# Kernel optimization log

Measured on AMD Instinct MI355X. Metric: run time of the kernel, lower is better.

Reference implementation:

```python
import jax, jax.numpy as jnp
import numpy as np

B, N, K, H = 4, 2048, 30, 128
NODE_IN, EDGE_IN, FF = 21, 16, 4 * H


def _normalize(t, axis=-1):
    d = t / jnp.linalg.norm(t, axis=axis, keepdims=True)
    return jnp.where(jnp.isnan(d), 0.0, d)


def gather_nodes(nodes, idx):
    # nodes: [B,N,C], idx: [B,N,K] -> [B,N,K,C]
    b, n, k = idx.shape
    flat = idx.reshape(b, n * k)
    out = jnp.take_along_axis(nodes, flat[:, :, None], axis=1)
    return out.reshape(b, n, k, nodes.shape[-1])


def cal_dihedral(Xf, eps=1e-7):
    dX = Xf[:, 1:, :] - Xf[:, :-1, :]
    U = _normalize(dX)
    u0, u1, u2 = U[:, :-2], U[:, 1:-1], U[:, 2:]
    n0 = _normalize(jnp.cross(u0, u1))
    n1 = _normalize(jnp.cross(u1, u2))
    cosD = jnp.clip((n0 * n1).sum(-1), -1 + eps, 1 - eps)
    v = _normalize(jnp.cross(n0, n1))
    return jnp.sign((-v * u1).sum(-1)) * jnp.arccos(cosD)


def dihedrals(X, eps=1e-7):
    b, n = X.shape[0], X.shape[1]
    Xf = X[:, :, :3, :].reshape(b, 3 * n, 3)
    D = cal_dihedral(Xf)
    D = jnp.pad(D, ((0, 0), (1, 2))).reshape(b, n, 3)
    dihed = jnp.concatenate([jnp.cos(D), jnp.sin(D)], -1)
    dX = Xf[:, 1:] - Xf[:, :-1]
    U = _normalize(dX)
    cosA = jnp.clip((U[:, :-2] * U[:, 1:-1]).sum(-1), -1 + eps, 1 - eps)
    A = jnp.pad(jnp.arccos(cosA), ((0, 0), (1, 2))).reshape(b, n, 3)
    ang = jnp.concatenate([jnp.cos(A), jnp.sin(A)], -1)
    return jnp.concatenate([dihed, ang], -1)  # [B,N,12]


def quaternions(R):
    diag = jnp.diagonal(R, axis1=-2, axis2=-1)
    Rxx, Ryy, Rzz = diag[..., 0], diag[..., 1], diag[..., 2]
    mags = 0.5 * jnp.sqrt(jnp.abs(1 + jnp.stack([Rxx - Ryy - Rzz, -Rxx + Ryy - Rzz, -Rxx - Ryy + Rzz], -1)))
    signs = jnp.sign(jnp.stack([R[..., 2, 1] - R[..., 1, 2], R[..., 0, 2] - R[..., 2, 0], R[..., 1, 0] - R[..., 0, 1]], -1))
    xyz = signs * mags
    w = jnp.sqrt(jax.nn.relu(1 + diag.sum(-1, keepdims=True))) / 2.0
    return _normalize(jnp.concatenate([xyz, w], -1))


def orientations(X, E_idx):
    V = X  # [B,N,4,3]
    b, n = X.shape[0], X.shape[1]
    k = E_idx.shape[2]
    Xf = X[:, :, :3, :].reshape(b, 3 * n, 3)
    dX = Xf[:, 1:] - Xf[:, :-1]
    U = _normalize(dX)
    u0, u1 = U[:, :-2], U[:, 1:-1]
    n0 = _normalize(jnp.cross(u0, u1))[:, ::3]
    b1 = _normalize(u0 - u1)[:, ::3]
    Xa = Xf[:, ::3]  # [B,N,3]
    Q = jnp.stack([b1, n0, jnp.cross(b1, n0)], 2)  # [B,N-1,3,3]
    Q = Q.reshape(b, Q.shape[1], 9)
    Q = jnp.pad(Q, ((0, 0), (0, 1), (0, 0)))  # [B,N,9]
    Qn = gather_nodes(Q, E_idx).reshape(b, n, k, 3, 3)
    Xn = gather_nodes(V[:, :, 1, :], E_idx)
    Nn = gather_nodes(V[:, :, 0, :], E_idx)
    Cn = gather_nodes(V[:, :, 2, :], E_idx)
    On = gather_nodes(V[:, :, 3, :], E_idx)
    Q3 = Q.reshape(b, n, 3, 3)
    dXn = jnp.stack([Xn, Nn, Cn, On], 3) - Xa[:, :, None, None, :]  # [B,N,K,4,3]
    dU = jnp.einsum('bnij,bnkaj->bnkai', Q3, dXn)
    E_direct = _normalize(dU).reshape(b, n, k, 12)
    R = jnp.einsum('bnji,bnkjl->bnkil', Q3, Qn)  # Q^T @ Q_neighbors
    q = quaternions(R)  # [B,N,K,4]
    dX_inner = V[:, :, jnp.array([0, 2, 3]), :] - Xa[:, :, None, :]
    dU_inner = _normalize(jnp.einsum('bnij,bnaj->bnai', Q3, dX_inner))
    V_direct = dU_inner.reshape(b, n, 9)
    return V_direct, E_direct, q


def layernorm(x, g, bta, eps=1e-5):
    m = x.mean(-1, keepdims=True)
    v = ((x - m) ** 2).mean(-1, keepdims=True)
    return (x - m) / jnp.sqrt(v + eps) * g + bta


def gelu(x):
    return jax.nn.gelu(x, approximate=False)


def forward(X, E_idx, Wv_w, Wv_b, We_w, We_b, W1_w, W1_b, W2_w, W2_b, W3_w, W3_b,
            Wi_w, Wi_b, Wo_w, Wo_b, ln1_g, ln1_b, ln2_g, ln2_b):
    k = E_idx.shape[2]
    Dfeat = dihedrals(X)                     # [B,N,12]
    Vd, Ed, q = orientations(X, E_idx)       # [B,N,9],[B,N,K,12],[B,N,K,4]
    hV = jnp.concatenate([Dfeat, Vd], -1) @ Wv_w + Wv_b     # [B,N,H]
    hE = jnp.concatenate([Ed, q], -1) @ We_w + We_b         # [B,N,K,H]
    hV_nbr = gather_nodes(hV, E_idx)                        # [B,N,K,H]
    hV_exp = jnp.broadcast_to(hV[:, :, None, :], hV_nbr.shape)
    hEV = jnp.concatenate([hV_exp, hE, hV_nbr], -1)         # [B,N,K,3H]
    msg = gelu(hEV @ W1_w + W1_b)
    msg = gelu(msg @ W2_w + W2_b)
    msg = msg @ W3_w + W3_b
    dh = msg.sum(-2) / k
    hV = layernorm(hV + dh, ln1_g, ln1_b)
    ff = gelu(hV @ Wi_w + Wi_b) @ Wo_w + Wo_b
    hV = layernorm(hV + ff, ln2_g, ln2_b)
    return hV


def _lin(key, fan_in, fan_out):
    s = 1.0 / np.sqrt(fan_in)
    kw, kb = jax.random.split(key)
    return (jax.random.uniform(kw, (fan_in, fan_out), minval=-s, maxval=s),
            jax.random.uniform(kb, (fan_out,), minval=-s, maxval=s))


def setup_inputs() -> dict:
    key = jax.random.key(0)
    ks = jax.random.split(key, 10)
    X = jax.random.normal(ks[0], (B, N, 4, 3), dtype=jnp.float32) * 3.0
    E_idx = jax.random.randint(ks[1], (B, N, K), 0, N)
    Wv_w, Wv_b = _lin(ks[2], NODE_IN, H)
    We_w, We_b = _lin(ks[3], EDGE_IN, H)
    W1_w, W1_b = _lin(ks[4], 3 * H, H)
    W2_w, W2_b = _lin(ks[5], H, H)
    W3_w, W3_b = _lin(ks[6], H, H)
    Wi_w, Wi_b = _lin(ks[7], H, FF)
    Wo_w, Wo_b = _lin(ks[8], FF, H)
    return {
        'X': X, 'E_idx': E_idx,
        'Wv_w': Wv_w, 'Wv_b': Wv_b, 'We_w': We_w, 'We_b': We_b,
        'W1_w': W1_w, 'W1_b': W1_b, 'W2_w': W2_w, 'W2_b': W2_b,
        'W3_w': W3_w, 'W3_b': W3_b, 'Wi_w': Wi_w, 'Wi_b': Wi_b,
        'Wo_w': Wo_w, 'Wo_b': Wo_b,
        'ln1_g': jnp.ones((H,), jnp.float32), 'ln1_b': jnp.zeros((H,), jnp.float32),
        'ln2_g': jnp.ones((H,), jnp.float32), 'ln2_b': jnp.zeros((H,), jnp.float32),
    }


def reference(X, E_idx, Wv_w, Wv_b, We_w, We_b, W1_w, W1_b, W2_w, W2_b, W3_w, W3_b,
              Wi_w, Wi_b, Wo_w, Wo_b, ln1_g, ln1_b, ln2_g, ln2_b):
    return forward(X, E_idx, Wv_w, Wv_b, We_w, We_b, W1_w, W1_b, W2_w, W2_b,
                   W3_w, W3_b, Wi_w, Wi_b, Wo_w, Wo_b, ln1_g, ln1_b, ln2_g, ln2_b)
```

## Files before the change

### kernel.cpp

```cpp
#include <hip/hip_runtime.h>
#include <math.h>

#define BB 4
#define NN 2048
#define KNB 30
#define HH 128
#define FFD 512

typedef __attribute__((ext_vector_type(4))) float  f32x4;
typedef __attribute__((ext_vector_type(8))) short  s16x8;
typedef __attribute__((ext_vector_type(4))) short  s16x4;

struct F3 { float x,y,z; };
__device__ __forceinline__ F3 f3(float a,float b,float c){ F3 r; r.x=a; r.y=b; r.z=c; return r; }
__device__ __forceinline__ F3 sub3(F3 a, F3 b){ return f3(a.x-b.x, a.y-b.y, a.z-b.z); }
__device__ __forceinline__ float dot3(F3 a, F3 b){ return a.x*b.x + a.y*b.y + a.z*b.z; }
__device__ __forceinline__ F3 cross3(F3 a, F3 b){
  return f3(a.y*b.z-a.z*b.y, a.z*b.x-a.x*b.z, a.x*b.y-a.y*b.x);
}
__device__ __forceinline__ F3 nrm3(F3 a){
  float n2 = dot3(a,a);
  if (n2 <= 0.f) return f3(0.f,0.f,0.f);
  float inv = 1.0f/sqrtf(n2);
  return f3(a.x*inv, a.y*inv, a.z*inv);
}
__device__ __forceinline__ float sgnf(float x){ return (x>0.f)?1.f:((x<0.f)?-1.f:0.f); }
__device__ __forceinline__ float clip1(float x){
  const float e = 1e-7f;
  return fminf(fmaxf(x, -1.f+e), 1.f-e);
}
__device__ __forceinline__ float fgelu(float x){
  float x2 = x*x;
  float t = __builtin_fmaf(-0.1029641763f, x2, -2.302344055f);
  float d = 1.f + __builtin_amdgcn_exp2f(t*x);
  return x * __builtin_amdgcn_rcpf(d);
}
__device__ __forceinline__ short f2bf(float x){
  union { float f; unsigned u; } v; v.f = x;
  unsigned r = v.u + 0x7fffu + ((v.u >> 16) & 1u);
  return (short)(r >> 16);
}

__global__ void k_init(const float* __restrict__ X, float* __restrict__ Qws,
                       float* __restrict__ featws,
                       const float* __restrict__ We, const float* __restrict__ Web,
                       const float* __restrict__ W1, const float* __restrict__ W2,
                       const float* __restrict__ Wi, const float* __restrict__ Wo,
                       const float* __restrict__ W3,
                       short* __restrict__ wfoldT, float* __restrict__ bfold,
                       short* __restrict__ w2t, short* __restrict__ w1aT,
                       short* __restrict__ w1cT, short* __restrict__ wiT,
                       short* __restrict__ woT, short* __restrict__ w3T){
  if (blockIdx.x < 32){
    int t = blockIdx.x*256 + threadIdx.x;
    int b = t / NN, n = t % NN;
    const float* Xb = X + (size_t)b*NN*12;
    #define LD3(r,a) f3(Xb[((r)*4+(a))*3+0], Xb[((r)*4+(a))*3+1], Xb[((r)*4+(a))*3+2])
    F3 x0=LD3(n,0), x1=LD3(n,1), x2=LD3(n,2), x3=LD3(n,3);
    F3 U[5];
    U[1]=nrm3(sub3(x1,x0));
    U[2]=nrm3(sub3(x2,x1));
    if (n>0){ F3 p = LD3(n-1,2); U[0]=nrm3(sub3(x0,p)); } else U[0]=f3(0.f,0.f,0.f);
    if (n<NN-1){ F3 y0=LD3(n+1,0), y1=LD3(n+1,1); U[3]=nrm3(sub3(y0,x2)); U[4]=nrm3(sub3(y1,y0)); }
    else { U[3]=f3(0.f,0.f,0.f); U[4]=f3(0.f,0.f,0.f); }

    float feat[21];
    #pragma unroll
    for (int tt=0; tt<3; tt++){
      bool valid = (n>0 || tt>0) && (n<NN-1 || tt==0);
      if (valid){
        F3 a=U[tt], bv=U[tt+1], c=U[tt+2];
        F3 n0=nrm3(cross3(a,bv)), n1=nrm3(cross3(bv,c));
        float cd = clip1(dot3(n0,n1));
        F3 v = nrm3(cross3(n0,n1));
        float s = sgnf(-dot3(v,bv));
        feat[tt]   = (s==0.f) ? 1.f : cd;
        feat[3+tt] = s*sqrtf(fmaxf(1.f-cd*cd, 0.f));
        float ca = clip1(dot3(a,bv));
        feat[6+tt] = ca;
        feat[9+tt] = sqrtf(fmaxf(1.f-ca*ca, 0.f));
      } else {
        feat[tt]=1.f; feat[3+tt]=0.f; feat[6+tt]=1.f; feat[9+tt]=0.f;
      }
    }
    float Q[9];
    if (n<NN-1){
      F3 b1=nrm3(sub3(U[1],U[2]));
      F3 n0=nrm3(cross3(U[1],U[2]));
      F3 r2=cross3(b1,n0);
      Q[0]=b1.x;Q[1]=b1.y;Q[2]=b1.z;Q[3]=n0.x;Q[4]=n0.y;Q[5]=n0.z;Q[6]=r2.x;Q[7]=r2.y;Q[8]=r2.z;
    } else {
      #pragma unroll
      for (int i=0;i<9;i++) Q[i]=0.f;
    }
    float* qp = Qws + (size_t)t*9;
    #pragma unroll
    for (int i=0;i<9;i++) qp[i]=Q[i];

    feat[12]=0.f; feat[13]=0.f; feat[14]=0.f;
    F3 d1=sub3(x2,x0), d2=sub3(x3,x0);
    F3 r1 = nrm3(f3(Q[0]*d1.x+Q[1]*d1.y+Q[2]*d1.z,
                    Q[3]*d1.x+Q[4]*d1.y+Q[5]*d1.z,
                    Q[6]*d1.x+Q[7]*d1.y+Q[8]*d1.z));
    F3 r2v= nrm3(f3(Q[0]*d2.x+Q[1]*d2.y+Q[2]*d2.z,
                    Q[3]*d2.x+Q[4]*d2.y+Q[5]*d2.z,
                    Q[6]*d2.x+Q[7]*d2.y+Q[8]*d2.z));
    feat[15]=r1.x; feat[16]=r1.y; feat[17]=r1.z;
    feat[18]=r2v.x; feat[19]=r2v.y; feat[20]=r2v.z;
    float* fp = featws + (size_t)t*21;
    #pragma unroll
    for (int i=0;i<21;i++) fp[i]=feat[i];
    #undef LD3
    return;
  }
  int t = (blockIdx.x-32)*256 + threadIdx.x;
  if (t < 2048){
    int c = t >> 4, j = t & 15;
    float a = 0.f;
    for (int k=0;k<HH;k++) a += We[j*HH+k]*W1[(HH+k)*HH + c];
    wfoldT[t] = f2bf(a);
  } else if (t < 2176){
    int c = t - 2048;
    float a = 0.f;
    for (int k=0;k<HH;k++) a += Web[k]*W1[(HH+k)*HH + c];
    bfold[c] = a;
  } else if (t < 18560){
    int i = t - 2176;  int n = i >> 7, k = i & 127;
    w2t[n*HH + k] = f2bf(W2[k*HH + n]);
  } else if (t < 34944){
    int i = t - 18560; int n = i >> 7, k = i & 127;
    w1aT[n*HH + k] = f2bf(W1[k*HH + n]);
  } else if (t < 51328){
    int i = t - 34944; int n = i >> 7, k = i & 127;
    w1cT[n*HH + k] = f2bf(W1[(256+k)*HH + n]);
  } else if (t < 116864){
    int i = t - 51328; int n = i >> 7, k = i & 127;
    wiT[n*HH + k] = f2bf(Wi[k*FFD + n]);
  } else if (t < 182400){
    int i = t - 116864; int k = i >> 7, n = i & 127;
    woT[n*FFD + k] = f2bf(Wo[k*HH + n]);
  } else if (t < 198784){
    int i = t - 182400; int n = i >> 7, k = i & 127;
    w3T[n*HH + k] = f2bf(W3[k*HH + n]);
  }
}

#define PNB 32
__global__ void k_pre(const float* __restrict__ featws, const float* __restrict__ Wv,
                      const float* __restrict__ Wvb, const short* __restrict__ w1aT,
                      const short* __restrict__ w1cT, const float* __restrict__ W1b,
                      const float* __restrict__ bfold, float* __restrict__ hVws,
                      float* __restrict__ Sws, float* __restrict__ Gws){
  __shared__ __align__(16) short hvL[PNB][136];
  int tid = threadIdx.x;
  int base = blockIdx.x*PNB;
  {
    int c = tid & 127, half = tid >> 7;
    float wv[21];
    #pragma unroll
    for (int j=0;j<21;j++) wv[j] = Wv[j*HH + c];
    float wb = Wvb[c];
    #pragma unroll 2
    for (int it=0; it<16; ++it){
      int g = it*2 + half;
      const float* f = featws + (size_t)(base+g)*21;
      float a = wb;
      #pragma unroll
      for (int j=0;j<21;j++) a += f[j]*wv[j];
      hVws[(size_t)(base+g)*HH + c] = a;
      hvL[g][c] = f2bf(a);
    }
  }
  __syncthreads();
  {
    int l = tid & 63, w = tid >> 6;
    int lr = l & 15, lg = l >> 4;
    int m = w & 1;
    int nbase = (w >> 1)*4;
    s16x8 afr[4];
    #pragma unroll
    for (int ks=0; ks<4; ks++)
      afr[ks] = *reinterpret_cast<const s16x8*>(&hvL[m*16 + lr][ks*32 + lg*8]);
    f32x4 Cs[4], Cg[4];
    #pragma unroll
    for (int q=0;q<4;q++){ Cs[q]=(f32x4){0,0,0,0}; Cg[q]=(f32x4){0,0,0,0}; }
    #pragma unroll
    for (int q=0;q<4;q++){
      int ncol = (nbase+q)*16 + lr;
      #pragma unroll
      for (int ks=0; ks<4; ks++){
        s16x8 ba = *reinterpret_cast<const s16x8*>(&w1aT[ncol*HH + ks*32 + lg*8]);
        s16x8 bc = *reinterpret_cast<const s16x8*>(&w1cT[ncol*HH + ks*32 + lg*8]);
        Cs[q] = __builtin_amdgcn_mfma_f32_16x16x32_bf16(afr[ks], ba, Cs[q], 0,0,0);
        Cg[q] = __builtin_amdgcn_mfma_f32_16x16x32_bf16(afr[ks], bc, Cg[q], 0,0,0);
      }
    }
    #pragma unroll
    for (int q=0;q<4;q++){
      int ncol = (nbase+q)*16 + lr;
      float bc = W1b[ncol] + bfold[ncol];
      #pragma unroll
      for (int i=0;i<4;i++){
        int row = m*16 + lg*4 + i;
        size_t o = (size_t)(base+row)*HH + ncol;
        Sws[o] = Cs[q][i] + bc;
        Gws[o] = Cg[q][i];
      }
    }
  }
}

#define NPB 4
#define A2STR 136
#define EFSTR 20
__launch_bounds__(256, 4)
__global__ void k_msg(const float* __restrict__ X, const int* __restrict__ Eidx,
                      const float* __restrict__ Qws, const float* __restrict__ Sws,
                      const float* __restrict__ Gws,
                      const short* __restrict__ wfoldT, const short* __restrict__ w2t,
                      const float* __restrict__ W2b, float* __restrict__ csws){
  __shared__ __align__(16) short efL[128*EFSTR];
  __shared__ int idxL[128];
  __shared__ __align__(16) short A2s[128*A2STR];

  const int tid = threadIdx.x;
  const int gbase = blockIdx.x*NPB;
  const int b = gbase >> 11;
  const int bofs = b*NN;

  if (tid < NPB*KNB){
    int nn = tid / KNB;
    int kk = tid - nn*KNB;
    int gnode = gbase + nn;
    int n = gnode - bofs;
    int j = Eidx[(size_t)gnode*KNB + kk];
    int r = nn*32 + kk;
    idxL[r] = j;
    const float* Qs = Qws + (size_t)gnode*9;
    float q[9];
    #pragma unroll
    for (int i=0;i<9;i++) q[i]=Qs[i];
    const float* Xb = X + (size_t)b*NN*12;
    F3 Xa = f3(Xb[n*12+0], Xb[n*12+1], Xb[n*12+2]);
    const float* Xn = Xb + (size_t)j*12;
    F3 A[4];
    A[0] = f3(Xn[3],  Xn[4],  Xn[5]);
    A[1] = f3(Xn[0],  Xn[1],  Xn[2]);
    A[2] = f3(Xn[6],  Xn[7],  Xn[8]);
    A[3] = f3(Xn[9],  Xn[10], Xn[11]);
    #pragma unroll
    for (int a=0;a<4;a++){
      F3 d = sub3(A[a], Xa);
      F3 w = f3(q[0]*d.x+q[1]*d.y+q[2]*d.z,
                q[3]*d.x+q[4]*d.y+q[5]*d.z,
                q[6]*d.x+q[7]*d.y+q[8]*d.z);
      F3 wn = nrm3(w);
      efL[r*EFSTR + a*3 + 0] = f2bf(wn.x);
      efL[r*EFSTR + a*3 + 1] = f2bf(wn.y);
      efL[r*EFSTR + a*3 + 2] = f2bf(wn.z);
    }
    const float* Qn = Qws + (size_t)(bofs + j)*9;
    float p[9];
    #pragma unroll
    for (int i=0;i<9;i++) p[i]=Qn[i];
    float R00=q[0]*p[0]+q[3]*p[3]+q[6]*p[6];
    float R01=q[0]*p[1]+q[3]*p[4]+q[6]*p[7];
    float R02=q[0]*p[2]+q[3]*p[5]+q[6]*p[8];
    float R10=q[1]*p[0]+q[4]*p[3]+q[7]*p[6];
    float R11=q[1]*p[1]+q[4]*p[4]+q[7]*p[7];
    float R12=q[1]*p[2]+q[4]*p[5]+q[7]*p[8];
    float R20=q[2]*p[0]+q[5]*p[3]+q[8]*p[6];
    float R21=q[2]*p[1]+q[5]*p[4]+q[8]*p[7];
    float R22=q[2]*p[2]+q[5]*p[5]+q[8]*p[8];
    float mx = 0.5f*sqrtf(fabsf(1.f+R00-R11-R22));
    float my = 0.5f*sqrtf(fabsf(1.f-R00+R11-R22));
    float mz = 0.5f*sqrtf(fabsf(1.f-R00-R11+R22));
    float qx = sgnf(R21-R12)*mx;
    float qy = sgnf(R02-R20)*my;
    float qz = sgnf(R10-R01)*mz;
    float qw = 0.5f*sqrtf(fmaxf(1.f+R00+R11+R22, 0.f));
    float n2 = qx*qx+qy*qy+qz*qz+qw*qw;
    float inv = (n2>0.f) ? 1.f/sqrtf(n2) : 0.f;
    efL[r*EFSTR+12]=f2bf(qx*inv); efL[r*EFSTR+13]=f2bf(qy*inv);
    efL[r*EFSTR+14]=f2bf(qz*inv); efL[r*EFSTR+15]=f2bf(qw*inv);
  } else if (tid < 128){
    int e = tid - 120;
    int nn = e >> 1, slot = 30 + (e & 1);
    int r = nn*32 + slot;
    idxL[r] = 0;
    #pragma unroll
    for (int j2=0;j2<16;j2++) efL[r*EFSTR + j2] = 0;
  }
  __syncthreads();

  const int w  = tid >> 6;
  const int l  = tid & 63;
  const int lr = l & 15;
  const int lg = l >> 4;

  {
    s16x8 wf[8];
    #pragma unroll
    for (int ct=0; ct<8; ct++){
      if (lg < 2)
        wf[ct] = *reinterpret_cast<const s16x8*>(&wfoldT[(ct*16+lr)*16 + lg*8]);
      else
        wf[ct] = (s16x8){0,0,0,0,0,0,0,0};
    }
    s16x8 ef[2];
    #pragma unroll
    for (int rt=0; rt<2; rt++){
      if (lg < 2){
        const short* p = &efL[(w*32 + rt*16 + lr)*EFSTR + lg*8];
        s16x4 lo = *reinterpret_cast<const s16x4*>(p);
        s16x4 hi = *reinterpret_cast<const s16x4*>(p+4);
        s16x8 v;
        #pragma unroll
        for (int j2=0;j2<4;j2++){ v[j2]=lo[j2]; v[4+j2]=hi[j2]; }
        ef[rt] = v;
      } else {
        ef[rt] = (s16x8){0,0,0,0,0,0,0,0};
      }
    }
    const int e0 = w*32 + lr;
    const int e1 = e0 + 16;
    const bool ok1 = (lr < KNB - 16);
    const float* g0 = Gws + (size_t)(bofs + idxL[e0])*HH;
    const float* g1 = Gws + (size_t)(bofs + idxL[e1])*HH;
    const float* Srow = Sws + (size_t)(gbase+w)*HH;
    #pragma unroll
    for (int ct=0; ct<8; ct++){
      const int cbase = ct*16 + lg*4;
      f32x4 S4 = *reinterpret_cast<const f32x4*>(Srow + cbase);
      f32x4 G0 = *reinterpret_cast<const f32x4*>(g0 + cbase);
      f32x4 G1 = *reinterpret_cast<const f32x4*>(g1 + cbase);
      f32x4 C0 = __builtin_amdgcn_mfma_f32_16x16x32_bf16(wf[ct], ef[0], (f32x4){0,0,0,0}, 0,0,0);
      f32x4 C1 = __builtin_amdgcn_mfma_f32_16x16x32_bf16(wf[ct], ef[1], (f32x4){0,0,0,0}, 0,0,0);
      s16x4 o0, o1;
      #pragma unroll
      for (int i=0;i<4;i++){
        o0[i] = f2bf(fgelu(C0[i] + S4[i] + G0[i]));
        float v1 = fgelu(C1[i] + S4[i] + G1[i]);
        o1[i] = ok1 ? f2bf(v1) : (short)0;
      }
      *reinterpret_cast<s16x4*>(&A2s[e0*A2STR + cbase]) = o0;
      *reinterpret_cast<s16x4*>(&A2s[e1*A2STR + cbase]) = o1;
    }
  }
  __syncthreads();

  {
    f32x4 Cacc[2][8];
    #pragma unroll
    for (int mt=0; mt<2; mt++)
      #pragma unroll
      for (int nt=0; nt<8; nt++)
        Cacc[mt][nt] = (f32x4){0.f,0.f,0.f,0.f};
    #pragma unroll
    for (int ks=0; ks<4; ks++){
      const int koff = ks*32 + lg*8;
      s16x8 a0 = *reinterpret_cast<const s16x8*>(&A2s[(w*32      + lr)*A2STR + koff]);
      s16x8 a1 = *reinterpret_cast<const s16x8*>(&A2s[(w*32 + 16 + lr)*A2STR + koff]);
      #pragma unroll
      for (int nt=0; nt<8; nt++){
        s16x8 bv = *reinterpret_cast<const s16x8*>(&w2t[(lr + nt*16)*HH + koff]);
        Cacc[0][nt] = __builtin_amdgcn_mfma_f32_16x16x32_bf16(a0, bv, Cacc[0][nt], 0,0,0);
        Cacc[1][nt] = __builtin_amdgcn_mfma_f32_16x16x32_bf16(a1, bv, Cacc[1][nt], 0,0,0);
      }
    }
    float* csrow = csws + (size_t)(gbase+w)*HH;
    #pragma unroll
    for (int nt=0; nt<8; nt++){
      float b2v = W2b[lr + nt*16];
      float part = 0.f;
      #pragma unroll
      for (int mt=0; mt<2; mt++){
        #pragma unroll
        for (int i=0; i<4; i++){
          int row32 = mt*16 + lg*4 + i;
          float v = fgelu(Cacc[mt][nt][i] + b2v);
          if (row32 < KNB) part += v;
        }
      }
      part += __shfl_xor(part, 16, 64);
      part += __shfl_xor(part, 32, 64);
      if (l < 16) csrow[nt*16 + lr] = part;
    }
  }
}

#define FNB 16
__global__ void k_ffn(const float* __restrict__ csws, const float* __restrict__ hVws,
                      const short* __restrict__ w3T, const float* __restrict__ W3b,
                      const short* __restrict__ wiT, const short* __restrict__ woT,
                      const float* __restrict__ Wib, const float* __restrict__ Wob,
                      const float* __restrict__ l1g, const float* __restrict__ l1b,
                      const float* __restrict__ l2g, const float* __restrict__ l2b,
                      float* __restrict__ out){
  __shared__ __align__(16) short hv1[FNB][136];
  __shared__ __align__(16) float yL[FNB][HH];
  __shared__ __align__(16) short ffh[FNB][520];
  __shared__ float partS[FNB][4], partQ[FNB][4];
  const int tid = threadIdx.x;
  const int l = tid & 63, w = tid >> 6;
  const int base = blockIdx.x*FNB;
  const int lr = l & 15, lg = l >> 4;

  {
    int i0 = tid*8;
    int row = i0 >> 7, col = i0 & 127;
    const float* p = csws + (size_t)(base+row)*HH + col;
    f32x4 a = *reinterpret_cast<const f32x4*>(p);
    f32x4 bq = *reinterpret_cast<const f32x4*>(p+4);
    s16x8 v;
    #pragma unroll
    for (int j=0;j<4;j++){ v[j]=f2bf(a[j]); v[4+j]=f2bf(bq[j]); }
    *reinterpret_cast<s16x8*>(&hv1[row][col]) = v;
  }
  __syncthreads();

  {
    s16x8 acs[4];
    #pragma unroll
    for (int ks=0; ks<4; ks++)
      acs[ks] = *reinterpret_cast<const s16x8*>(&hv1[lr][ks*32 + lg*8]);
    f32x4 Cd[2];
    Cd[0]=(f32x4){0,0,0,0}; Cd[1]=(f32x4){0,0,0,0};
    #pragma unroll
    for (int t2=0; t2<2; t2++){
      int ncol = (2*w+t2)*16 + lr;
      #pragma unroll
      for (int ks=0; ks<4; ks++){
        s16x8 bv = *reinterpret_cast<const s16x8*>(&w3T[ncol*HH + ks*32 + lg*8]);
        Cd[t2] = __builtin_amdgcn_mfma_f32_16x16x32_bf16(acs[ks], bv, Cd[t2], 0,0,0);
      }
    }
    float vv[2][4];
    float ps[4] = {0,0,0,0}, pq[4] = {0,0,0,0};
    #pragma unroll
    for (int t2=0; t2<2; t2++){
      int col = (2*w+t2)*16 + lr;
      float b3 = W3b[col];
      #pragma unroll
      for (int i=0;i<4;i++){
        int row = lg*4 + i;
        float v = hVws[(size_t)(base+row)*HH + col] + Cd[t2][i]*(1.f/30.f) + b3;
        vv[t2][i] = v;
        ps[i] += v; pq[i] += v*v;
      }
    }
    #pragma unroll
    for (int i=0;i<4;i++){
      #pragma unroll
      for (int o=1;o<16;o<<=1){
        ps[i] += __shfl_xor(ps[i], o, 64);
        pq[i] += __shfl_xor(pq[i], o, 64);
      }
      if (lr == 0){ partS[lg*4+i][w] = ps[i]; partQ[lg*4+i][w] = pq[i]; }
    }
    __syncthreads();
    #pragma unroll
    for (int t2=0; t2<2; t2++){
      int col = (2*w+t2)*16 + lr;
      float g1 = l1g[col], b1 = l1b[col];
      #pragma unroll
      for (int i=0;i<4;i++){
        int row = lg*4 + i;
        float S = partS[row][0]+partS[row][1]+partS[row][2]+partS[row][3];
        float Q = partQ[row][0]+partQ[row][1]+partQ[row][2]+partQ[row][3];
        float m = S*(1.f/HH);
        float inv = 1.f/sqrtf(Q*(1.f/HH) - m*m + 1e-5f);
        float y = (vv[t2][i]-m)*inv*g1 + b1;
        yL[row][col] = y;
        hv1[row][col] = f2bf(y);
      }
    }
  }
  __syncthreads();

  {
    s16x8 afr[4];
    #pragma unroll
    for (int ks=0; ks<4; ks++)
      afr[ks] = *reinterpret_cast<const s16x8*>(&hv1[lr][ks*32 + lg*8]);
    #pragma unroll
    for (int q=0; q<8; q++){
      int ncol = (w*8+q)*16 + lr;
      f32x4 C = (f32x4){0,0,0,0};
      #pragma unroll
      for (int ks=0; ks<4; ks++){
        s16x8 bv = *reinterpret_cast<const s16x8*>(&wiT[ncol*HH + ks*32 + lg*8]);
        C = __builtin_amdgcn_mfma_f32_16x16x32_bf16(afr[ks], bv, C, 0,0,0);
      }
      float bi = Wib[ncol];
      #pragma unroll
      for (int i=0;i<4;i++){
        int row = lg*4 + i;
        ffh[row][ncol] = f2bf(fgelu(C[i] + bi));
      }
    }
  }
  __syncthreads();

  f32x4 C2[2];
  C2[0]=(f32x4){0,0,0,0}; C2[1]=(f32x4){0,0,0,0};
  for (int ks=0; ks<16; ++ks){
    s16x8 a = *reinterpret_cast<const s16x8*>(&ffh[lr][ks*32 + lg*8]);
    #pragma unroll
    for (int t2=0; t2<2; t2++){
      int ncol = (2*w+t2)*16 + lr;
      s16x8 bv = *reinterpret_cast<const s16x8*>(&woT[ncol*FFD + ks*32 + lg*8]);
      C2[t2] = __builtin_amdgcn_mfma_f32_16x16x32_bf16(a, bv, C2[t2], 0,0,0);
    }
  }
  float vv[2][4];
  float ps[4] = {0,0,0,0}, pq[4] = {0,0,0,0};
  #pragma unroll
  for (int t2=0; t2<2; t2++){
    int col = (2*w+t2)*16 + lr;
    float bo = Wob[col];
    #pragma unroll
    for (int i=0;i<4;i++){
      int row = lg*4 + i;
      float v = yL[row][col] + C2[t2][i] + bo;
      vv[t2][i] = v;
      ps[i] += v; pq[i] += v*v;
    }
  }
  #pragma unroll
  for (int i=0;i<4;i++){
    #pragma unroll
    for (int o=1;o<16;o<<=1){
      ps[i] += __shfl_xor(ps[i], o, 64);
      pq[i] += __shfl_xor(pq[i], o, 64);
    }
    if (lr == 0){ partS[lg*4+i][w] = ps[i]; partQ[lg*4+i][w] = pq[i]; }
  }
  __syncthreads();
  float mean[4], inv[4];
  #pragma unroll
  for (int i=0;i<4;i++){
    int row = lg*4 + i;
    float S = partS[row][0]+partS[row][1]+partS[row][2]+partS[row][3];
    float Q = partQ[row][0]+partQ[row][1]+partQ[row][2]+partQ[row][3];
    float m = S*(1.f/HH);
    float var = Q*(1.f/HH) - m*m;
    mean[i] = m;
    inv[i] = 1.f/sqrtf(var + 1e-5f);
  }
  #pragma unroll
  for (int t2=0; t2<2; t2++){
    int col = (2*w+t2)*16 + lr;
    float g2 = l2g[col], b2 = l2b[col];
    #pragma unroll
    for (int i=0;i<4;i++){
      int row = lg*4 + i;
      out[(size_t)(base+row)*HH + col] = (vv[t2][i]-mean[i])*inv[i]*g2 + b2;
    }
  }
}

extern "C" void kernel_launch(void* const* d_in, const int* in_sizes, int n_in,
                              void* d_out, int out_size, void* d_ws, size_t ws_size,
                              hipStream_t stream) {
  (void)in_sizes; (void)n_in; (void)out_size; (void)ws_size;
  const float* X   = (const float*)d_in[0];
  const int*   Ei  = (const int*)  d_in[1];
  const float* Wv  = (const float*)d_in[2];
  const float* Wvb = (const float*)d_in[3];
  const float* We  = (const float*)d_in[4];
  const float* Web = (const float*)d_in[5];
  const float* W1  = (const float*)d_in[6];
  const float* W1b = (const float*)d_in[7];
  const float* W2  = (const float*)d_in[8];
  const float* W2b = (const float*)d_in[9];
  const float* W3  = (const float*)d_in[10];
  const float* W3b = (const float*)d_in[11];
  const float* Wi  = (const float*)d_in[12];
  const float* Wib = (const float*)d_in[13];
  const float* Wo  = (const float*)d_in[14];
  const float* Wob = (const float*)d_in[15];
  const float* l1g = (const float*)d_in[16];
  const float* l1b = (const float*)d_in[17];
  const float* l2g = (const float*)d_in[18];
  const float* l2b = (const float*)d_in[19];
  float* out = (float*)d_out;

  float* wsf    = (float*)d_ws;
  float* featws = wsf + 0;
  float* Qws    = wsf + 172032;
  float* hVws   = wsf + 245760;
  float* Gws    = wsf + 1294336;
  float* Sws    = wsf + 2342912;
  float* csws   = wsf + 3391488;
  short* wfoldT = (short*)(wsf + 4440064);
  float* bfold  = wsf + 4441088;
  short* w2t    = (short*)(wsf + 4441216);
  short* w1aT   = (short*)(wsf + 4449408);
  short* w1cT   = (short*)(wsf + 4457600);
  short* wiT    = (short*)(wsf + 4465792);
  short* woT    = (short*)(wsf + 4498560);
  short* w3T    = (short*)(wsf + 4531328);

  k_init<<<dim3(809), dim3(256), 0, stream>>>(X, Qws, featws, We, Web, W1, W2, Wi, Wo, W3,
                                              wfoldT, bfold, w2t, w1aT, w1cT, wiT, woT, w3T);
  k_pre <<<dim3(BB*NN/PNB), dim3(256), 0, stream>>>(featws, Wv, Wvb, w1aT, w1cT,
                                                    W1b, bfold, hVws, Sws, Gws);
  k_msg <<<dim3(BB*NN/NPB), dim3(256), 0, stream>>>(X, Ei, Qws, Sws, Gws,
                                                    wfoldT, w2t, W2b, csws);
  k_ffn <<<dim3(BB*NN/FNB), dim3(256), 0, stream>>>(csws, hVws, w3T, W3b, wiT, woT,
                                                    Wib, Wob, l1g, l1b, l2g, l2b, out);
}
```

Baseline: 192.6 us.

## Split edge feature computation out of message kernel into separate k_edge kernel

Moves the per-edge geometric feature computation (relative directions and quaternion) from k_msg into a new k_edge kernel that uses all 256 threads per block and writes bf16 edge features to a global buffer. In the old k_msg only 120 of 256 threads did this scalar work before a barrier while the rest idled. k_msg now loads the edge features and neighbour indices straight from global memory and drops its small LDS arrays and the barrier. The cost is an extra kernel launch plus a global write and read of about 4 MB of edge features.

```diff
diff --git a/kernel.cpp b/kernel.cpp
--- a/kernel.cpp
+++ b/kernel.cpp
@@ -145,97 +145,18 @@
   }
 }
 
-#define PNB 32
-__global__ void k_pre(const float* __restrict__ featws, const float* __restrict__ Wv,
-                      const float* __restrict__ Wvb, const short* __restrict__ w1aT,
-                      const short* __restrict__ w1cT, const float* __restrict__ W1b,
-                      const float* __restrict__ bfold, float* __restrict__ hVws,
-                      float* __restrict__ Sws, float* __restrict__ Gws){
-  __shared__ __align__(16) short hvL[PNB][136];
-  int tid = threadIdx.x;
-  int base = blockIdx.x*PNB;
-  {
-    int c = tid & 127, half = tid >> 7;
-    float wv[21];
-    #pragma unroll
-    for (int j=0;j<21;j++) wv[j] = Wv[j*HH + c];
-    float wb = Wvb[c];
-    #pragma unroll 2
-    for (int it=0; it<16; ++it){
-      int g = it*2 + half;
-      const float* f = featws + (size_t)(base+g)*21;
-      float a = wb;
-      #pragma unroll
-      for (int j=0;j<21;j++) a += f[j]*wv[j];
-      hVws[(size_t)(base+g)*HH + c] = a;
-      hvL[g][c] = f2bf(a);
-    }
-  }
-  __syncthreads();
-  {
-    int l = tid & 63, w = tid >> 6;
-    int lr = l & 15, lg = l >> 4;
-    int m = w & 1;
-    int nbase = (w >> 1)*4;
-    s16x8 afr[4];
-    #pragma unroll
-    for (int ks=0; ks<4; ks++)
-      afr[ks] = *reinterpret_cast<const s16x8*>(&hvL[m*16 + lr][ks*32 + lg*8]);
-    f32x4 Cs[4], Cg[4];
-    #pragma unroll
-    for (int q=0;q<4;q++){ Cs[q]=(f32x4){0,0,0,0}; Cg[q]=(f32x4){0,0,0,0}; }
-    #pragma unroll
-    for (int q=0;q<4;q++){
-      int ncol = (nbase+q)*16 + lr;
-      #pragma unroll
-      for (int ks=0; ks<4; ks++){
-        s16x8 ba = *reinterpret_cast<const s16x8*>(&w1aT[ncol*HH + ks*32 + lg*8]);
-        s16x8 bc = *reinterpret_cast<const s16x8*>(&w1cT[ncol*HH + ks*32 + lg*8]);
-        Cs[q] = __builtin_amdgcn_mfma_f32_16x16x32_bf16(afr[ks], ba, Cs[q], 0,0,0);
-        Cg[q] = __builtin_amdgcn_mfma_f32_16x16x32_bf16(afr[ks], bc, Cg[q], 0,0,0);
-      }
-    }
-    #pragma unroll
-    for (int q=0;q<4;q++){
-      int ncol = (nbase+q)*16 + lr;
-      float bc = W1b[ncol] + bfold[ncol];
-      #pragma unroll
-      for (int i=0;i<4;i++){
-        int row = m*16 + lg*4 + i;
-        size_t o = (size_t)(base+row)*HH + ncol;
-        Sws[o] = Cs[q][i] + bc;
-        Gws[o] = Cg[q][i];
-      }
-    }
-  }
-}
-
-#define NPB 4
-#define A2STR 136
-#define EFSTR 20
-__launch_bounds__(256, 4)
-__global__ void k_msg(const float* __restrict__ X, const int* __restrict__ Eidx,
-                      const float* __restrict__ Qws, const float* __restrict__ Sws,
-                      const float* __restrict__ Gws,
-                      const short* __restrict__ wfoldT, const short* __restrict__ w2t,
-                      const float* __restrict__ W2b, float* __restrict__ csws){
-  __shared__ __align__(16) short efL[128*EFSTR];
-  __shared__ int idxL[128];
-  __shared__ __align__(16) short A2s[128*A2STR];
-
+#define ENB 8
+__global__ void k_edge(const float* __restrict__ X, const int* __restrict__ Eidx,
+                       const float* __restrict__ Qws, short* __restrict__ efB){
   const int tid = threadIdx.x;
-  const int gbase = blockIdx.x*NPB;
-  const int b = gbase >> 11;
+  const int nn = tid >> 5, slot = tid & 31;
+  const int gnode = blockIdx.x*ENB + nn;
+  const int b = gnode >> 11;
+  const int n = gnode & (NN-1);
   const int bofs = b*NN;
-
-  if (tid < NPB*KNB){
-    int nn = tid / KNB;
-    int kk = tid - nn*KNB;
-    int gnode = gbase + nn;
-    int n = gnode - bofs;
-    int j = Eidx[(size_t)gnode*KNB + kk];
-    int r = nn*32 + kk;
-    idxL[r] = j;
+  short out[16];
+  if (slot < KNB){
+    int j = Eidx[(size_t)gnode*KNB + slot];
     const float* Qs = Qws + (size_t)gnode*9;
     float q[9];
     #pragma unroll
@@ -255,9 +176,9 @@
                 q[3]*d.x+q[4]*d.y+q[5]*d.z,
                 q[6]*d.x+q[7]*d.y+q[8]*d.z);
       F3 wn = nrm3(w);
-      efL[r*EFSTR + a*3 + 0] = f2bf(wn.x);
-      efL[r*EFSTR + a*3 + 1] = f2bf(wn.y);
-      efL[r*EFSTR + a*3 + 2] = f2bf(wn.z);
+      out[a*3+0] = f2bf(wn.x);
+      out[a*3+1] = f2bf(wn.y);
+      out[a*3+2] = f2bf(wn.z);
     }
     const float* Qn = Qws + (size_t)(bofs + j)*9;
     float p[9];
@@ -281,22 +202,101 @@
     float qw = 0.5f*sqrtf(fmaxf(1.f+R00+R11+R22, 0.f));
     float n2 = qx*qx+qy*qy+qz*qz+qw*qw;
     float inv = (n2>0.f) ? 1.f/sqrtf(n2) : 0.f;
-    efL[r*EFSTR+12]=f2bf(qx*inv); efL[r*EFSTR+13]=f2bf(qy*inv);
-    efL[r*EFSTR+14]=f2bf(qz*inv); efL[r*EFSTR+15]=f2bf(qw*inv);
-  } else if (tid < 128){
-    int e = tid - 120;
-    int nn = e >> 1, slot = 30 + (e & 1);
-    int r = nn*32 + slot;
-    idxL[r] = 0;
-    #pragma unroll
-    for (int j2=0;j2<16;j2++) efL[r*EFSTR + j2] = 0;
+    out[12]=f2bf(qx*inv); out[13]=f2bf(qy*inv);
+    out[14]=f2bf(qz*inv); out[15]=f2bf(qw*inv);
+  } else {
+    #pragma unroll
+    for (int i=0;i<16;i++) out[i]=0;
+  }
+  short* dst = efB + ((size_t)gnode*32 + slot)*16;
+  *reinterpret_cast<s16x8*>(dst)   = *reinterpret_cast<s16x8*>(&out[0]);
+  *reinterpret_cast<s16x8*>(dst+8) = *reinterpret_cast<s16x8*>(&out[8]);
+}
+
+#define PNB 32
+__global__ void k_pre(const float* __restrict__ featws, const float* __restrict__ Wv,
+                      const float* __restrict__ Wvb, const short* __restrict__ w1aT,
+                      const short* __restrict__ w1cT, const float* __restrict__ W1b,
+                      const float* __restrict__ bfold, float* __restrict__ hVws,
+                      float* __restrict__ Sws, float* __restrict__ Gws){
+  __shared__ __align__(16) short hvL[PNB][136];
+  int tid = threadIdx.x;
+  int base = blockIdx.x*PNB;
+  {
+    int c = tid & 127, half = tid >> 7;
+    float wv[21];
+    #pragma unroll
+    for (int j=0;j<21;j++) wv[j] = Wv[j*HH + c];
+    float wb = Wvb[c];
+    #pragma unroll 2
+    for (int it=0; it<16; ++it){
+      int g = it*2 + half;
+      const float* f = featws + (size_t)(base+g)*21;
+      float a = wb;
+      #pragma unroll
+      for (int j=0;j<21;j++) a += f[j]*wv[j];
+      hVws[(size_t)(base+g)*HH + c] = a;
+      hvL[g][c] = f2bf(a);
+    }
   }
   __syncthreads();
+  {
+    int l = tid & 63, w = tid >> 6;
+    int lr = l & 15, lg = l >> 4;
+    int m = w & 1;
+    int nbase = (w >> 1)*4;
+    s16x8 afr[4];
+    #pragma unroll
+    for (int ks=0; ks<4; ks++)
+      afr[ks] = *reinterpret_cast<const s16x8*>(&hvL[m*16 + lr][ks*32 + lg*8]);
+    f32x4 Cs[4], Cg[4];
+    #pragma unroll
+    for (int q=0;q<4;q++){ Cs[q]=(f32x4){0,0,0,0}; Cg[q]=(f32x4){0,0,0,0}; }
+    #pragma unroll
+    for (int q=0;q<4;q++){
+      int ncol = (nbase+q)*16 + lr;
+      #pragma unroll
+      for (int ks=0; ks<4; ks++){
+        s16x8 ba = *reinterpret_cast<const s16x8*>(&w1aT[ncol*HH + ks*32 + lg*8]);
+        s16x8 bc = *reinterpret_cast<const s16x8*>(&w1cT[ncol*HH + ks*32 + lg*8]);
+        Cs[q] = __builtin_amdgcn_mfma_f32_16x16x32_bf16(afr[ks], ba, Cs[q], 0,0,0);
+        Cg[q] = __builtin_amdgcn_mfma_f32_16x16x32_bf16(afr[ks], bc, Cg[q], 0,0,0);
+      }
+    }
+    #pragma unroll
+    for (int q=0;q<4;q++){
+      int ncol = (nbase+q)*16 + lr;
+      float bc = W1b[ncol] + bfold[ncol];
+      #pragma unroll
+      for (int i=0;i<4;i++){
+        int row = m*16 + lg*4 + i;
+        size_t o = (size_t)(base+row)*HH + ncol;
+        Sws[o] = Cs[q][i] + bc;
+        Gws[o] = Cg[q][i];
+      }
+    }
+  }
+}
+
+#define NPB 4
+#define A2STR 136
+__launch_bounds__(256, 4)
+__global__ void k_msg(const int* __restrict__ Eidx, const short* __restrict__ efB,
+                      const float* __restrict__ Sws, const float* __restrict__ Gws,
+                      const short* __restrict__ wfoldT, const short* __restrict__ w2t,
+                      const float* __restrict__ W2b, float* __restrict__ csws){
+  __shared__ __align__(16) short A2s[128*A2STR];
+
+  const int tid = threadIdx.x;
+  const int gbase = blockIdx.x*NPB;
+  const int b = gbase >> 11;
+  const int bofs = b*NN;
 
   const int w  = tid >> 6;
   const int l  = tid & 63;
   const int lr = l & 15;
   const int lg = l >> 4;
+  const int gnode = gbase + w;
 
   {
     s16x8 wf[8];
@@ -307,27 +307,23 @@
       else
         wf[ct] = (s16x8){0,0,0,0,0,0,0,0};
     }
+    const short* efn = efB + (size_t)gnode*32*16;
     s16x8 ef[2];
     #pragma unroll
     for (int rt=0; rt<2; rt++){
-      if (lg < 2){
-        const short* p = &efL[(w*32 + rt*16 + lr)*EFSTR + lg*8];
-        s16x4 lo = *reinterpret_cast<const s16x4*>(p);
-        s16x4 hi = *reinterpret_cast<const s16x4*>(p+4);
-        s16x8 v;
-        #pragma unroll
-        for (int j2=0;j2<4;j2++){ v[j2]=lo[j2]; v[4+j2]=hi[j2]; }
-        ef[rt] = v;
-      } else {
+      if (lg < 2)
+        ef[rt] = *reinterpret_cast<const s16x8*>(&efn[(rt*16 + lr)*16 + lg*8]);
+      else
         ef[rt] = (s16x8){0,0,0,0,0,0,0,0};
-      }
-    }
+    }
+    const bool ok1 = (lr < KNB - 16);
+    int j0 = Eidx[(size_t)gnode*KNB + lr];
+    int j1 = ok1 ? Eidx[(size_t)gnode*KNB + 16 + lr] : 0;
+    const float* g0 = Gws + (size_t)(bofs + j0)*HH;
+    const float* g1 = Gws + (size_t)(bofs + j1)*HH;
+    const float* Srow = Sws + (size_t)gnode*HH;
     const int e0 = w*32 + lr;
     const int e1 = e0 + 16;
-    const bool ok1 = (lr < KNB - 16);
-    const float* g0 = Gws + (size_t)(bofs + idxL[e0])*HH;
-    const float* g1 = Gws + (size_t)(bofs + idxL[e1])*HH;
-    const float* Srow = Sws + (size_t)(gbase+w)*HH;
     #pragma unroll
     for (int ct=0; ct<8; ct++){
       const int cbase = ct*16 + lg*4;
@@ -368,7 +364,7 @@
         Cacc[1][nt] = __builtin_amdgcn_mfma_f32_16x16x32_bf16(a1, bv, Cacc[1][nt], 0,0,0);
       }
     }
-    float* csrow = csws + (size_t)(gbase+w)*HH;
+    float* csrow = csws + (size_t)gnode*HH;
     #pragma unroll
     for (int nt=0; nt<8; nt++){
       float b2v = W2b[lr + nt*16];
@@ -593,20 +589,22 @@
   float* Gws    = wsf + 1294336;
   float* Sws    = wsf + 2342912;
   float* csws   = wsf + 3391488;
-  short* wfoldT = (short*)(wsf + 4440064);
-  float* bfold  = wsf + 4441088;
-  short* w2t    = (short*)(wsf + 4441216);
-  short* w1aT   = (short*)(wsf + 4449408);
-  short* w1cT   = (short*)(wsf + 4457600);
-  short* wiT    = (short*)(wsf + 4465792);
-  short* woT    = (short*)(wsf + 4498560);
-  short* w3T    = (short*)(wsf + 4531328);
+  short* efB    = (short*)(wsf + 4440064);
+  short* wfoldT = (short*)(wsf + 6537216);
+  float* bfold  = wsf + 6538240;
+  short* w2t    = (short*)(wsf + 6538368);
+  short* w1aT   = (short*)(wsf + 6546560);
+  short* w1cT   = (short*)(wsf + 6554752);
+  short* wiT    = (short*)(wsf + 6562944);
+  short* woT    = (short*)(wsf + 6595712);
+  short* w3T    = (short*)(wsf + 6628480);
 
   k_init<<<dim3(809), dim3(256), 0, stream>>>(X, Qws, featws, We, Web, W1, W2, Wi, Wo, W3,
                                               wfoldT, bfold, w2t, w1aT, w1cT, wiT, woT, w3T);
+  k_edge<<<dim3(BB*NN/ENB), dim3(256), 0, stream>>>(X, Ei, Qws, efB);
   k_pre <<<dim3(BB*NN/PNB), dim3(256), 0, stream>>>(featws, Wv, Wvb, w1aT, w1cT,
                                                     W1b, bfold, hVws, Sws, Gws);
-  k_msg <<<dim3(BB*NN/NPB), dim3(256), 0, stream>>>(X, Ei, Qws, Sws, Gws,
+  k_msg <<<dim3(BB*NN/NPB), dim3(256), 0, stream>>>(Ei, efB, Sws, Gws,
                                                     wfoldT, w2t, W2b, csws);
   k_ffn <<<dim3(BB*NN/FNB), dim3(256), 0, stream>>>(csws, hVws, w3T, W3b, wiT, woT,
                                                     Wib, Wob, l1g, l1b, l2g, l2b, out);
```

New measurement: 196.6 us. 2.1% more time.
